# Kernel tuning notes

Measured on AMD Instinct MI355X. Metric: run time of the kernel, lower is better.

## Reference

```python
import jax, jax.numpy as jnp
import numpy as np
from jax import lax

NB, HH, WW, C = 8, 64, 64, 192
G, K, DW_K, PA_K = 12, 3, 5, 3
GC, P = C // G, K * K
PAD, STRIDE, DIL = 1, 1, 1
OFFSET_SCALE = 1.0
LN_EPS = 1e-5


def _grid_sample(img, grid):
    # img: (B,Cc,H,W); grid: (B,L,P,2) xy in [-1,1]; bilinear, zeros padding, align_corners=False
    B, Cc, H, W = img.shape
    gx = (grid[..., 0] + 1.0) * (W * 0.5) - 0.5
    gy = (grid[..., 1] + 1.0) * (H * 0.5) - 0.5
    x0, y0 = jnp.floor(gx), jnp.floor(gy)

    def gather(xi, yi):
        valid = (xi >= 0) & (xi <= W - 1) & (yi >= 0) & (yi <= H - 1)
        xc = jnp.clip(xi, 0, W - 1).astype(jnp.int32)
        yc = jnp.clip(yi, 0, H - 1).astype(jnp.int32)
        v = jax.vmap(lambda im, y, x: im[:, y, x])(img, yc, xc)  # (B,Cc,L,P)
        return v * valid[:, None].astype(img.dtype)

    wx1, wy1 = gx - x0, gy - y0
    wx0, wy0 = 1.0 - wx1, 1.0 - wy1
    return (gather(x0, y0) * (wx0 * wy0)[:, None]
            + gather(x0 + 1.0, y0) * (wx1 * wy0)[:, None]
            + gather(x0, y0 + 1.0) * (wx0 * wy1)[:, None]
            + gather(x0 + 1.0, y0 + 1.0) * (wx1 * wy1)[:, None])


def _dcnv3_core(x, offset, mask):
    # x: (N,H,W,C) projected input; offset: (N,H,W,G*P*2); mask: (N,H,W,G*P)
    N, H, W, _ = x.shape
    xp = jnp.pad(x, ((0, 0), (PAD, PAD), (PAD, PAD), (0, 0)))
    Hp, Wp = H + 2 * PAD, W + 2 * PAD
    Ho, Wo = offset.shape[1], offset.shape[2]
    base = (DIL * (K - 1)) // 2 + 0.5
    ref_y = (base + jnp.arange(Ho) * STRIDE) / Hp
    ref_x = (base + jnp.arange(Wo) * STRIDE) / Wp
    ref = jnp.stack(jnp.broadcast_arrays(ref_x[None, :], ref_y[:, None]), -1)  # (Ho,Wo,2) xy
    start = -((DIL * (K - 1)) // 2)
    pts = (start + jnp.arange(K) * DIL).astype(x.dtype)
    gxg = jnp.broadcast_to((pts / Wp)[:, None], (K, K))  # w offset varies along dim0 (torch order)
    gyg = jnp.broadcast_to((pts / Hp)[None, :], (K, K))
    grid = jnp.tile(jnp.stack([gxg, gyg], -1).reshape(P, 2), (G, 1))  # (G*P,2)
    loc = ref[None, :, :, None, :] + grid * OFFSET_SCALE  # (1,Ho,Wo,G*P,2)
    norm = jnp.array([Wp, Hp], dtype=x.dtype)
    loc = loc + offset.reshape(N, Ho, Wo, G * P, 2) * OFFSET_SCALE / norm
    sg = 2.0 * loc - 1.0  # (N,Ho,Wo,G*P,2)
    img = xp.reshape(N, Hp * Wp, G, GC).transpose(0, 2, 3, 1).reshape(N * G, GC, Hp, Wp)
    grd = sg.reshape(N, Ho * Wo, G, P, 2).transpose(0, 2, 1, 3, 4).reshape(N * G, Ho * Wo, P, 2)
    samp = _grid_sample(img, grd)  # (N*G, GC, L, P)
    m = mask.reshape(N, Ho * Wo, G, P).transpose(0, 2, 1, 3).reshape(N * G, 1, Ho * Wo, P)
    out = (samp * m).sum(-1)  # (N*G, GC, L)
    return out.reshape(N, G, GC, Ho * Wo).transpose(0, 3, 1, 2).reshape(N, Ho, Wo, C)


def _dcnv3(x, dw_w, dw_b, ln_g, ln_b, off_w, off_b, msk_w, msk_b, in_w, in_b, out_w, out_b, cfs_w, cfs_b):
    N, H, W, _ = x.shape
    x_proj = x @ in_w + in_b
    # depthwise conv (5x5) -> LayerNorm (channels_last) -> GELU(exact)
    u = lax.conv_general_dilated(x, dw_w, (1, 1), 'SAME',
                                 dimension_numbers=('NHWC', 'HWIO', 'NHWC'),
                                 feature_group_count=C) + dw_b
    mu = u.mean(-1, keepdims=True)
    var = ((u - mu) ** 2).mean(-1, keepdims=True)
    u = (u - mu) * lax.rsqrt(var + LN_EPS) * ln_g + ln_b
    u = jax.nn.gelu(u, approximate=False)
    offset = u @ off_w + off_b  # (N,H,W,G*P*2)
    m = jax.nn.softmax((u @ msk_w + msk_b).reshape(N, H, W, G, P), axis=-1).reshape(N, H, W, G * P)
    y = _dcnv3_core(x_proj, offset, m)
    cfs = jax.nn.sigmoid(u @ cfs_w + cfs_b)  # (N,H,W,G)
    cfs = jnp.repeat(cfs, GC, axis=-1)       # (N,H,W,C), group-blockwise
    y = y * (1.0 - cfs) + x_proj * cfs
    return y @ out_w + out_b


def _patch_attention(x):
    # x: (N,H,W,C) -> std over softmax'd 3x3 neighbor scores: (N,H,W)
    N, H, W, _ = x.shape
    pad = (PA_K - 1) // 2
    xp = jnp.pad(x, ((0, 0), (pad, pad), (pad, pad), (0, 0)))
    neigh = jnp.stack([xp[:, i:i + H, j:j + W, :] for i in range(PA_K) for j in range(PA_K)],
                      axis=-1)  # (N,H,W,C,K1*K2), torch unfold ordering
    scores = jnp.einsum('nhwc,nhwck->nhwk', x, neigh)
    sm = jax.nn.softmax(scores, axis=-1)
    return jnp.std(sm, axis=-1, ddof=1)  # torch.std is unbiased


def setup_inputs() -> dict:
    key = jax.random.key(0)
    ks = jax.random.split(key, 8)
    s = 0.02
    return {
        'x': jax.random.normal(ks[0], (NB, HH, WW, C), jnp.float32),
        'dw_w': jax.random.normal(ks[1], (DW_K, DW_K, 1, C), jnp.float32) * s,
        'dw_b': jnp.zeros((C,), jnp.float32),
        'ln_g': jnp.ones((C,), jnp.float32),
        'ln_b': jnp.zeros((C,), jnp.float32),
        'off_w': jax.random.normal(ks[2], (C, G * P * 2), jnp.float32) * s,
        'off_b': jnp.zeros((G * P * 2,), jnp.float32),
        'msk_w': jax.random.normal(ks[3], (C, G * P), jnp.float32) * s,
        'msk_b': jnp.zeros((G * P,), jnp.float32),
        'in_w': jax.random.normal(ks[4], (C, C), jnp.float32) * s,
        'in_b': jnp.zeros((C,), jnp.float32),
        'out_w': jax.random.normal(ks[5], (C, C), jnp.float32) * s,
        'out_b': jnp.zeros((C,), jnp.float32),
        'cfs_w': jax.random.normal(ks[6], (C, G), jnp.float32) * s,
        'cfs_b': jnp.zeros((G,), jnp.float32),
    }


def reference(x, dw_w, dw_b, ln_g, ln_b, off_w, off_b, msk_w, msk_b, in_w, in_b, out_w, out_b, cfs_w, cfs_b):
    x1 = _dcnv3(x, dw_w, dw_b, ln_g, ln_b, off_w, off_b, msk_w, msk_b, in_w, in_b, out_w, out_b, cfs_w, cfs_b)
    mask = _patch_attention(x1)           # (N,H,W)
    return x + x1 * mask[..., None]
```

## Files before the change

### kernel.cpp

```cpp
#include <hip/hip_runtime.h>
#include <hip/hip_bf16.h>
#include <math.h>

#define NB 8
#define HH 64
#define WW 64
#define C 192
#define G 12
#define GC 16
#define P 9
#define NPIX (NB*HH*WW)

typedef __attribute__((ext_vector_type(8))) short short8;
typedef __attribute__((ext_vector_type(4))) float f32x4;
typedef unsigned short ushort;

__device__ __forceinline__ ushort to_bf16(float f) {
  __hip_bfloat16 b = __float2bfloat16(f);
  return *(ushort*)&b;
}
__device__ __forceinline__ float bf2f(ushort u) {
  union { unsigned u; float f; } cv; cv.u = ((unsigned)u) << 16; return cv.f;
}
__device__ __forceinline__ float bflo(unsigned u) {
  union { unsigned v; float f; } c; c.v = u << 16; return c.f;
}
__device__ __forceinline__ float bfhi(unsigned u) {
  union { unsigned v; float f; } c; c.v = u & 0xffff0000u; return c.f;
}

__global__ void prep_w_kernel(const float* __restrict__ in_w, const float* __restrict__ out_w,
    const float* __restrict__ off_w, const float* __restrict__ msk_w, const float* __restrict__ cfs_w,
    const float* __restrict__ off_b, const float* __restrict__ msk_b, const float* __restrict__ cfs_b,
    ushort* __restrict__ in_wt, ushort* __restrict__ out_wt, ushort* __restrict__ wf_t,
    float* __restrict__ bf_bias) {
  int idx = blockIdx.x*256 + threadIdx.x;
  if (idx < 36864) {
    int n = idx/192, k = idx%192;
    in_wt[idx] = to_bf16(in_w[k*192 + n]);
  } else if (idx < 73728) {
    int j = idx - 36864; int n = j/192, k = j%192;
    out_wt[j] = to_bf16(out_w[k*192 + n]);
  } else if (idx < 147456) {
    int j = idx - 73728; int n = j/192, k = j%192;
    float v = 0.f;
    if (n < 216)      v = off_w[k*216 + n];
    else if (n < 324) v = msk_w[k*108 + (n-216)];
    else if (n < 336) v = cfs_w[k*12  + (n-324)];
    wf_t[j] = to_bf16(v);
  }
  if (idx < 384) {
    float b = 0.f;
    if (idx < 216)      b = off_b[idx];
    else if (idx < 324) b = msk_b[idx-216];
    else if (idx < 336) b = cfs_b[idx-324];
    bf_bias[idx] = b;
  }
}

template<int NW, int NSTORE, bool BF16OUT, bool AF32>
__global__ __launch_bounds__(256) void mfma_gemm(const void* __restrict__ A_,
    const ushort* __restrict__ Wt, const float* __restrict__ bias,
    void* __restrict__ Cout_) {
  __shared__ ushort As[4*128*8];
  __shared__ ushort Bs[4*64*8];
  int pix0 = blockIdx.x * 128, n0 = blockIdx.y * 64;
  int tid = threadIdx.x;
  int wid = tid >> 6, lane = tid & 63;
  int lr = lane >> 4, lc = lane & 15;

  f32x4 acc[2][4];
  #pragma unroll
  for (int m=0;m<2;m++)
    #pragma unroll
    for (int j=0;j<4;j++) acc[m][j] = (f32x4){0.f,0.f,0.f,0.f};

  int sa0_kb = tid >> 7,        sa0_row = tid & 127;
  int sa1_kb = (tid+256) >> 7,  sa1_row = (tid+256) & 127;
  int sb_kb  = tid >> 6,        sb_n    = tid & 63;

  short8 pa0, pa1, pb;
  auto load_tile = [&](int k0) {
    if (AF32) {
      const float* Af = (const float*)A_;
      float4 u0 = *(const float4*)&Af[(size_t)(pix0 + sa0_row)*192 + k0 + sa0_kb*8];
      float4 u1 = *(const float4*)&Af[(size_t)(pix0 + sa0_row)*192 + k0 + sa0_kb*8 + 4];
      pa0[0]=to_bf16(u0.x); pa0[1]=to_bf16(u0.y); pa0[2]=to_bf16(u0.z); pa0[3]=to_bf16(u0.w);
      pa0[4]=to_bf16(u1.x); pa0[5]=to_bf16(u1.y); pa0[6]=to_bf16(u1.z); pa0[7]=to_bf16(u1.w);
      float4 v0 = *(const float4*)&Af[(size_t)(pix0 + sa1_row)*192 + k0 + sa1_kb*8];
      float4 v1 = *(const float4*)&Af[(size_t)(pix0 + sa1_row)*192 + k0 + sa1_kb*8 + 4];
      pa1[0]=to_bf16(v0.x); pa1[1]=to_bf16(v0.y); pa1[2]=to_bf16(v0.z); pa1[3]=to_bf16(v0.w);
      pa1[4]=to_bf16(v1.x); pa1[5]=to_bf16(v1.y); pa1[6]=to_bf16(v1.z); pa1[7]=to_bf16(v1.w);
    } else {
      const ushort* Ab = (const ushort*)A_;
      pa0 = *(const short8*)&Ab[(size_t)(pix0 + sa0_row)*192 + k0 + sa0_kb*8];
      pa1 = *(const short8*)&Ab[(size_t)(pix0 + sa1_row)*192 + k0 + sa1_kb*8];
    }
    pb  = *(const short8*)&Wt[(size_t)(n0 + sb_n)*192 + k0 + sb_kb*8];
  };
  load_tile(0);

  for (int t = 0; t < 6; t++) {
    __syncthreads();
    *(short8*)&As[(size_t)tid*8]        = pa0;
    *(short8*)&As[(size_t)(tid+256)*8]  = pa1;
    *(short8*)&Bs[(size_t)tid*8]        = pb;
    __syncthreads();
    if (t < 5) load_tile((t+1)*32);
    short8 a0 = *(const short8*)&As[(size_t)(lr*128 + wid*32 + lc)*8];
    short8 a1 = *(const short8*)&As[(size_t)(lr*128 + wid*32 + 16 + lc)*8];
    #pragma unroll
    for (int j=0;j<4;j++) {
      short8 b = *(const short8*)&Bs[(size_t)(lr*64 + j*16 + lc)*8];
      acc[0][j] = __builtin_amdgcn_mfma_f32_16x16x32_bf16(a0, b, acc[0][j], 0,0,0);
      acc[1][j] = __builtin_amdgcn_mfma_f32_16x16x32_bf16(a1, b, acc[1][j], 0,0,0);
    }
  }
  #pragma unroll
  for (int j=0;j<4;j++) {
    int col = n0 + j*16 + lc;
    if (NW != NSTORE && col >= NSTORE) continue;
    float bb = bias[col];
    #pragma unroll
    for (int m=0;m<2;m++) {
      size_t rbase = pix0 + wid*32 + m*16 + lr*4;
      #pragma unroll
      for (int r=0;r<4;r++) {
        float v = acc[m][j][r] + bb;
        if (BF16OUT) ((ushort*)Cout_)[(rbase + r)*NSTORE + col] = to_bf16(v);
        else         ((float*) Cout_)[(rbase + r)*NSTORE + col] = v;
      }
    }
  }
}

#define SEG 16
__global__ __launch_bounds__(192) void dw_ln_gelu_kernel(const float* __restrict__ x,
    const float* __restrict__ dw_w, const float* __restrict__ dw_b,
    const float* __restrict__ ln_g, const float* __restrict__ ln_b,
    ushort* __restrict__ u_out) {
  int blk = blockIdx.x;
  int qw = blk & 3; int nh = blk >> 2;
  int h = nh & 63, n = nh >> 6;
  int c = threadIdx.x;
  int w0 = qw * SEG;

  float kw[25];
  #pragma unroll
  for (int t=0;t<25;t++) kw[t] = dw_w[t*C + c];

  float acc[SEG];
  float bb = dw_b[c];
  #pragma unroll
  for (int i=0;i<SEG;i++) acc[i] = bb;

  #pragma unroll
  for (int i=0;i<5;i++) {
    int hy = h + i - 2;
    if (hy < 0 || hy >= HH) continue;
    const float* rowp = &x[(((size_t)n*HH + hy)*WW)*C + c];
    #pragma unroll
    for (int wi=0; wi<SEG+4; wi++) {
      int w_in = w0 - 2 + wi;
      if (w_in < 0 || w_in >= WW) continue;
      float v = rowp[(size_t)w_in*C];
      #pragma unroll
      for (int j=0;j<5;j++) {
        int a = wi - j;
        if (a >= 0 && a < SEG) acc[a] += v * kw[i*5+j];
      }
    }
  }

  __shared__ float lds_acc[SEG][C+1];
  __shared__ float part1[SEG][12], part2[SEG][12];
  __shared__ float mu_s[SEG], rs_s[SEG];
  #pragma unroll
  for (int i=0;i<SEG;i++) lds_acc[i][c] = acc[i];
  __syncthreads();
  {
    int p = threadIdx.x & 15, chunk = threadIdx.x >> 4;
    float s1 = 0.f, s2 = 0.f;
    #pragma unroll
    for (int k=0;k<16;k++) {
      float v = lds_acc[p][chunk*16 + k];
      s1 += v; s2 += v*v;
    }
    part1[p][chunk] = s1; part2[p][chunk] = s2;
  }
  __syncthreads();
  if (threadIdx.x < SEG) {
    int p = threadIdx.x;
    float t1 = 0.f, t2 = 0.f;
    #pragma unroll
    for (int k=0;k<12;k++){ t1 += part1[p][k]; t2 += part2[p][k]; }
    float mu = t1 * (1.0f/C);
    float var = t2 * (1.0f/C) - mu*mu;
    mu_s[p] = mu; rs_s[p] = rsqrtf(var + 1e-5f);
  }
  __syncthreads();
  float gg = ln_g[c], lb = ln_b[c];
  size_t obase = ((size_t)nh*WW + w0)*C + c;
  #pragma unroll
  for (int i=0;i<SEG;i++) {
    float uv = (acc[i] - mu_s[i])*rs_s[i]*gg + lb;
    uv = 0.5f*uv*(1.0f + erff(uv*0.70710678118654752f));
    u_out[obase + (size_t)i*C] = to_bf16(uv);
  }
}

#define SPX 8
__device__ __forceinline__ void fma8(float* acc, float w, uint4 q) {
  acc[0] += w*bflo(q.x); acc[1] += w*bfhi(q.x);
  acc[2] += w*bflo(q.y); acc[3] += w*bfhi(q.y);
  acc[4] += w*bflo(q.z); acc[5] += w*bfhi(q.z);
  acc[6] += w*bflo(q.w); acc[7] += w*bfhi(q.w);
}
__global__ __launch_bounds__(192) void sample_kernel(const ushort* __restrict__ omc,
    const ushort* __restrict__ x_proj, ushort* __restrict__ y_out) {
  int pix0 = blockIdx.x * SPX;
  int n = pix0 >> 12;
  int hw = pix0 & 4095; int h = hw >> 6; int w0 = hw & 63;
  int tid = threadIdx.x;
  __shared__ int   addrs[SPX*108*4];
  __shared__ float wts[SPX*108*4];
  __shared__ float msm[SPX][108];
  __shared__ float cfss[SPX][12];

  for (int i = tid; i < SPX*108; i += 192) {
    int px = i / 108, gp = i % 108;
    int p = gp % 9;
    const float pts[3] = {-1.f, 0.f, 1.f};
    unsigned off2 = ((const unsigned*)omc)[(size_t)(pix0+px)*168 + gp];
    float ox = bflo(off2), oy = bfhi(off2);
    float gx = 1.0f + (float)(w0+px) + pts[p/3] + ox;
    float gy = 1.0f + (float)h + pts[p%3] + oy;
    float x0f = floorf(gx), y0f = floorf(gy);
    float wx1 = gx - x0f, wy1 = gy - y0f;
    float wx0 = 1.f-wx1, wy0 = 1.f-wy1;
    int x0 = (int)x0f, y0 = (int)y0f;
    bool xv0 = (x0   >= 1) && (x0   <= 64);
    bool xv1 = (x0+1 >= 1) && (x0+1 <= 64);
    bool yv0 = (y0   >= 1) && (y0   <= 64);
    bool yv1 = (y0+1 >= 1) && (y0+1 <= 64);
    int base = n*HH*WW*C;
    int4 a4;
    a4.x = (yv0&&xv0) ? (base + ((y0-1)*WW + (x0-1))*C)*2 : 0;
    a4.y = (yv0&&xv1) ? (base + ((y0-1)*WW + (x0  ))*C)*2 : 0;
    a4.z = (yv1&&xv0) ? (base + ((y0  )*WW + (x0-1))*C)*2 : 0;
    a4.w = (yv1&&xv1) ? (base + ((y0  )*WW + (x0  ))*C)*2 : 0;
    ((int4*)addrs)[i] = a4;
    float4 w4;
    w4.x = (yv0&&xv0) ? wx0*wy0 : 0.f;
    w4.y = (yv0&&xv1) ? wx1*wy0 : 0.f;
    w4.z = (yv1&&xv0) ? wx0*wy1 : 0.f;
    w4.w = (yv1&&xv1) ? wx1*wy1 : 0.f;
    ((float4*)wts)[i] = w4;
  }
  if (tid < SPX*12) {
    int px = tid / 12, gg = tid % 12;
    const ushort* mrow = &omc[(size_t)(pix0+px)*336 + 216 + gg*9];
    float lv[P];
    #pragma unroll
    for (int p=0;p<P;p++) lv[p] = bf2f(mrow[p]);
    float m = -1e30f;
    #pragma unroll
    for (int p=0;p<P;p++) m = fmaxf(m, lv[p]);
    float e[P]; float s = 0.f;
    #pragma unroll
    for (int p=0;p<P;p++){ e[p] = expf(lv[p]-m); s += e[p]; }
    float inv = 1.0f/s;
    #pragma unroll
    for (int p=0;p<P;p++) msm[px][gg*9+p] = e[p]*inv;
  } else {
    int q = tid - SPX*12;
    int px = q / 12, gg = q % 12;
    cfss[px][gg] = 1.0f/(1.0f+expf(-bf2f(omc[(size_t)(pix0+px)*336 + 324 + gg])));
  }
  __syncthreads();
  for (int i = tid; i < SPX*108; i += 192) {
    int px = i / 108, gp = i % 108;
    float m = msm[px][gp] * (1.0f - cfss[px][gp/9]);
    f32x4 w4 = *(f32x4*)&wts[i*4];
    w4 *= m;
    *(f32x4*)&wts[i*4] = w4;
  }
  __syncthreads();
  int px = tid / 24, s = tid - (tid/24)*24;
  int g = s >> 1;
  int cb = s * 16;
  const char* xb = (const char*)x_proj;
  float acc[8] = {0.f,0.f,0.f,0.f,0.f,0.f,0.f,0.f};
  #pragma unroll
  for (int pb = 0; pb < 3; pb++) {
    int gp = g*9 + pb*3;
    int4 a0 = ((const int4*)addrs)[px*108+gp];
    int4 a1 = ((const int4*)addrs)[px*108+gp+1];
    int4 a2 = ((const int4*)addrs)[px*108+gp+2];
    float4 wv0 = ((const float4*)wts)[px*108+gp];
    float4 wv1 = ((const float4*)wts)[px*108+gp+1];
    float4 wv2 = ((const float4*)wts)[px*108+gp+2];
    uint4 t00 = *(const uint4*)(xb + (unsigned)(a0.x + cb));
    uint4 t01 = *(const uint4*)(xb + (unsigned)(a0.y + cb));
    uint4 t02 = *(const uint4*)(xb + (unsigned)(a0.z + cb));
    uint4 t03 = *(const uint4*)(xb + (unsigned)(a0.w + cb));
    uint4 t10 = *(const uint4*)(xb + (unsigned)(a1.x + cb));
    uint4 t11 = *(const uint4*)(xb + (unsigned)(a1.y + cb));
    uint4 t12 = *(const uint4*)(xb + (unsigned)(a1.z + cb));
    uint4 t13 = *(const uint4*)(xb + (unsigned)(a1.w + cb));
    uint4 t20 = *(const uint4*)(xb + (unsigned)(a2.x + cb));
    uint4 t21 = *(const uint4*)(xb + (unsigned)(a2.y + cb));
    uint4 t22 = *(const uint4*)(xb + (unsigned)(a2.z + cb));
    uint4 t23 = *(const uint4*)(xb + (unsigned)(a2.w + cb));
    fma8(acc, wv0.x, t00); fma8(acc, wv0.y, t01);
    fma8(acc, wv0.z, t02); fma8(acc, wv0.w, t03);
    fma8(acc, wv1.x, t10); fma8(acc, wv1.y, t11);
    fma8(acc, wv1.z, t12); fma8(acc, wv1.w, t13);
    fma8(acc, wv2.x, t20); fma8(acc, wv2.y, t21);
    fma8(acc, wv2.z, t22); fma8(acc, wv2.w, t23);
  }
  float cf = cfss[px][g];
  uint4 qx = *(const uint4*)(xb + ((size_t)(pix0+px)*C)*2 + cb);
  fma8(acc, cf, qx);
  short8 r;
  #pragma unroll
  for (int k=0;k<8;k++) r[k] = to_bf16(acc[k]);
  *(short8*)&y_out[(size_t)(pix0+px)*C + s*8] = r;
}

__global__ __launch_bounds__(256) void pattn_kernel(const float* __restrict__ x,
    const ushort* __restrict__ x1, float* __restrict__ out) {
  __shared__ unsigned xs[100*97];
  __shared__ float psc[64][36];
  __shared__ float sd_s[64];
  int blk = blockIdx.x;
  int n = blk >> 6;
  int ty = (blk >> 3) & 7, tx = blk & 7;
  int th0 = ty*8, tw0 = tx*8;
  int tid = threadIdx.x;
  const unsigned* x1u = (const unsigned*)x1;
  for (int i = tid; i < 100*96; i += 256) {
    int cell = i / 96, wd = i - cell*96;
    int gy = th0 - 1 + cell/10, gx = tw0 - 1 + cell%10;
    unsigned v = 0;
    if (gy>=0 && gy<HH && gx>=0 && gx<WW)
      v = x1u[(((size_t)n*HH+gy)*WW+gx)*96 + wd];
    xs[cell*97 + wd] = v;
  }
  __syncthreads();
  {
    int px = tid >> 2, qq = tid & 3;
    int py = px >> 3, pxx = px & 7;
    int cell = (py+1)*10 + (pxx+1);
    float cen[48];
    #pragma unroll
    for (int k=0;k<24;k++) {
      unsigned w = xs[cell*97 + qq*24 + k];
      cen[2*k] = bflo(w); cen[2*k+1] = bfhi(w);
    }
    #pragma unroll
    for (int ni=0;ni<9;ni++) {
      int nc = cell + (ni/3-1)*10 + (ni%3-1);
      float a = 0.f;
      #pragma unroll
      for (int k=0;k<24;k++) {
        unsigned w = xs[nc*97 + qq*24 + k];
        a += cen[2*k]*bflo(w) + cen[2*k+1]*bfhi(w);
      }
      psc[px][qq*9+ni] = a;
    }
  }
  __syncthreads();
  if (tid < 64) {
    float sc[9];
    #pragma unroll
    for (int k=0;k<9;k++)
      sc[k] = psc[tid][k] + psc[tid][9+k] + psc[tid][18+k] + psc[tid][27+k];
    float m = sc[0];
    #pragma unroll
    for (int k=1;k<9;k++) m = fmaxf(m, sc[k]);
    float pr[9]; float s = 0.f;
    #pragma unroll
    for (int k=0;k<9;k++){ pr[k] = expf(sc[k]-m); s += pr[k]; }
    float inv = 1.0f/s;
    float mean = 0.f;
    #pragma unroll
    for (int k=0;k<9;k++){ pr[k] *= inv; mean += pr[k]; }
    mean *= (1.0f/9.0f);
    float var = 0.f;
    #pragma unroll
    for (int k=0;k<9;k++){ float d = pr[k]-mean; var += d*d; }
    sd_s[tid] = sqrtf(var*(1.0f/8.0f));
  }
  __syncthreads();
  for (int i = tid; i < 64*96; i += 256) {
    int p2 = i / 96, wd = i - p2*96;
    int py2 = p2 >> 3, px2 = p2 & 7;
    unsigned v = xs[((py2+1)*10 + (px2+1))*97 + wd];
    size_t pix = ((size_t)n*HH + th0+py2)*WW + tw0+px2;
    float2 xv = ((const float2*)x)[pix*96 + wd];
    float sd = sd_s[p2];
    float2 o; o.x = xv.x + bflo(v)*sd; o.y = xv.y + bfhi(v)*sd;
    ((float2*)out)[pix*96 + wd] = o;
  }
}

extern "C" void kernel_launch(void* const* d_in, const int* in_sizes, int n_in,
                              void* d_out, int out_size, void* d_ws, size_t ws_size,
                              hipStream_t stream) {
  const float* x     = (const float*)d_in[0];
  const float* dw_w  = (const float*)d_in[1];
  const float* dw_b  = (const float*)d_in[2];
  const float* ln_g  = (const float*)d_in[3];
  const float* ln_b  = (const float*)d_in[4];
  const float* off_w = (const float*)d_in[5];
  const float* off_b = (const float*)d_in[6];
  const float* msk_w = (const float*)d_in[7];
  const float* msk_b = (const float*)d_in[8];
  const float* in_w  = (const float*)d_in[9];
  const float* in_b  = (const float*)d_in[10];
  const float* out_w = (const float*)d_in[11];
  const float* out_b = (const float*)d_in[12];
  const float* cfs_w = (const float*)d_in[13];
  const float* cfs_b = (const float*)d_in[14];
  float* outp = (float*)d_out;

  ushort* omc    = (ushort*)d_ws;
  ushort* xproj  = omc + (size_t)NPIX*336;
  ushort* x1_bf  = xproj + (size_t)NPIX*192;
  ushort* u_bf   = x1_bf + (size_t)NPIX*192;
  ushort* in_wt  = u_bf + (size_t)NPIX*192;
  ushort* out_wt = in_wt + 192*192;
  ushort* wf_t   = out_wt + 192*192;
  float*  bfb    = (float*)(wf_t + 384*192);

  prep_w_kernel<<<(147456+255)/256, 256, 0, stream>>>(in_w, out_w, off_w, msk_w, cfs_w,
                                                       off_b, msk_b, cfs_b,
                                                       in_wt, out_wt, wf_t, bfb);
  mfma_gemm<192,192,true,true><<<dim3(NPIX/128, 3), 256, 0, stream>>>(x, in_wt, in_b, xproj);
  dw_ln_gelu_kernel<<<NB*HH*4, 192, 0, stream>>>(x, dw_w, dw_b, ln_g, ln_b, u_bf);
  mfma_gemm<384,336,true,false><<<dim3(NPIX/128, 6), 256, 0, stream>>>(u_bf, wf_t, bfb, omc);
  sample_kernel<<<NPIX/SPX, 192, 0, stream>>>(omc, xproj, u_bf);
  mfma_gemm<192,192,true,false><<<dim3(NPIX/128, 3), 256, 0, stream>>>(u_bf, out_wt, out_b, x1_bf);
  pattn_kernel<<<NB*64, 256, 0, stream>>>(x, x1_bf, outp);
}
```

Baseline: 155.3 us.

## Stage 8x8 tile halo of projected input in LDS for deformable sampling

The sampling kernel now works on 8x8 pixel tiles. Each block first loads a 12x12 halo of x_proj for all channels into shared memory, and the bilinear corner taps are read from there whenever they land inside the halo. Taps outside the halo fall back to global loads. Offset decoding, the mask softmax and the sigmoid weight are fused into the per-thread loop, which removes the separate shared-memory address and weight tables and two barriers. The cost is a large LDS footprint and a smaller grid (512 blocks), which may limit occupancy. It also adds a divergent fallback path when offsets are large.

```diff
diff --git a/kernel.cpp b/kernel.cpp
--- a/kernel.cpp
+++ b/kernel.cpp
@@ -209,123 +209,118 @@
   }
 }
 
-#define SPX 8
-__device__ __forceinline__ void fma8(float* acc, float w, uint4 q) {
-  acc[0] += w*bflo(q.x); acc[1] += w*bfhi(q.x);
-  acc[2] += w*bflo(q.y); acc[3] += w*bfhi(q.y);
-  acc[4] += w*bflo(q.z); acc[5] += w*bfhi(q.z);
-  acc[6] += w*bflo(q.w); acc[7] += w*bfhi(q.w);
-}
-__global__ __launch_bounds__(192) void sample_kernel(const ushort* __restrict__ omc,
+#define CELLB 400
+__device__ __forceinline__ void fma16(float* acc, float wv, uint4 q0, uint4 q1) {
+  acc[0] += wv*bflo(q0.x); acc[1] += wv*bfhi(q0.x);
+  acc[2] += wv*bflo(q0.y); acc[3] += wv*bfhi(q0.y);
+  acc[4] += wv*bflo(q0.z); acc[5] += wv*bfhi(q0.z);
+  acc[6] += wv*bflo(q0.w); acc[7] += wv*bfhi(q0.w);
+  acc[8]  += wv*bflo(q1.x); acc[9]  += wv*bfhi(q1.x);
+  acc[10] += wv*bflo(q1.y); acc[11] += wv*bfhi(q1.y);
+  acc[12] += wv*bflo(q1.z); acc[13] += wv*bfhi(q1.z);
+  acc[14] += wv*bflo(q1.w); acc[15] += wv*bfhi(q1.w);
+}
+__global__ __launch_bounds__(256) void sample_kernel(const ushort* __restrict__ omc,
     const ushort* __restrict__ x_proj, ushort* __restrict__ y_out) {
-  int pix0 = blockIdx.x * SPX;
-  int n = pix0 >> 12;
-  int hw = pix0 & 4095; int h = hw >> 6; int w0 = hw & 63;
+  __shared__ uint4 xs4[144*CELLB/16];
+  char* xs = (char*)xs4;
+  int blk = blockIdx.x;
+  int n = blk >> 6, ty = (blk >> 3) & 7, tx = blk & 7;
+  int h0 = ty*8, w0 = tx*8;
   int tid = threadIdx.x;
-  __shared__ int   addrs[SPX*108*4];
-  __shared__ float wts[SPX*108*4];
-  __shared__ float msm[SPX][108];
-  __shared__ float cfss[SPX][12];
-
-  for (int i = tid; i < SPX*108; i += 192) {
-    int px = i / 108, gp = i % 108;
-    int p = gp % 9;
-    const float pts[3] = {-1.f, 0.f, 1.f};
-    unsigned off2 = ((const unsigned*)omc)[(size_t)(pix0+px)*168 + gp];
-    float ox = bflo(off2), oy = bfhi(off2);
-    float gx = 1.0f + (float)(w0+px) + pts[p/3] + ox;
-    float gy = 1.0f + (float)h + pts[p%3] + oy;
-    float x0f = floorf(gx), y0f = floorf(gy);
-    float wx1 = gx - x0f, wy1 = gy - y0f;
-    float wx0 = 1.f-wx1, wy0 = 1.f-wy1;
-    int x0 = (int)x0f, y0 = (int)y0f;
-    bool xv0 = (x0   >= 1) && (x0   <= 64);
-    bool xv1 = (x0+1 >= 1) && (x0+1 <= 64);
-    bool yv0 = (y0   >= 1) && (y0   <= 64);
-    bool yv1 = (y0+1 >= 1) && (y0+1 <= 64);
-    int base = n*HH*WW*C;
-    int4 a4;
-    a4.x = (yv0&&xv0) ? (base + ((y0-1)*WW + (x0-1))*C)*2 : 0;
-    a4.y = (yv0&&xv1) ? (base + ((y0-1)*WW + (x0  ))*C)*2 : 0;
-    a4.z = (yv1&&xv0) ? (base + ((y0  )*WW + (x0-1))*C)*2 : 0;
-    a4.w = (yv1&&xv1) ? (base + ((y0  )*WW + (x0  ))*C)*2 : 0;
-    ((int4*)addrs)[i] = a4;
-    float4 w4;
-    w4.x = (yv0&&xv0) ? wx0*wy0 : 0.f;
-    w4.y = (yv0&&xv1) ? wx1*wy0 : 0.f;
-    w4.z = (yv1&&xv0) ? wx0*wy1 : 0.f;
-    w4.w = (yv1&&xv1) ? wx1*wy1 : 0.f;
-    ((float4*)wts)[i] = w4;
-  }
-  if (tid < SPX*12) {
-    int px = tid / 12, gg = tid % 12;
-    const ushort* mrow = &omc[(size_t)(pix0+px)*336 + 216 + gg*9];
-    float lv[P];
-    #pragma unroll
-    for (int p=0;p<P;p++) lv[p] = bf2f(mrow[p]);
-    float m = -1e30f;
-    #pragma unroll
-    for (int p=0;p<P;p++) m = fmaxf(m, lv[p]);
-    float e[P]; float s = 0.f;
-    #pragma unroll
-    for (int p=0;p<P;p++){ e[p] = expf(lv[p]-m); s += e[p]; }
-    float inv = 1.0f/s;
-    #pragma unroll
-    for (int p=0;p<P;p++) msm[px][gg*9+p] = e[p]*inv;
-  } else {
-    int q = tid - SPX*12;
-    int px = q / 12, gg = q % 12;
-    cfss[px][gg] = 1.0f/(1.0f+expf(-bf2f(omc[(size_t)(pix0+px)*336 + 324 + gg])));
-  }
-  __syncthreads();
-  for (int i = tid; i < SPX*108; i += 192) {
-    int px = i / 108, gp = i % 108;
-    float m = msm[px][gp] * (1.0f - cfss[px][gp/9]);
-    f32x4 w4 = *(f32x4*)&wts[i*4];
-    w4 *= m;
-    *(f32x4*)&wts[i*4] = w4;
-  }
-  __syncthreads();
-  int px = tid / 24, s = tid - (tid/24)*24;
-  int g = s >> 1;
-  int cb = s * 16;
+
+  for (int i = tid; i < 144*24; i += 256) {
+    int cell = i / 24, k = i - cell*24;
+    int r = cell / 12, c = cell - r*12;
+    int y_u = h0 + r - 2, x_u = w0 + c - 2;
+    uint4 v = {0u,0u,0u,0u};
+    if ((unsigned)y_u < 64u && (unsigned)x_u < 64u)
+      v = *(const uint4*)&x_proj[((size_t)n*4096 + y_u*64 + x_u)*192 + k*8];
+    *(uint4*)&xs[cell*CELLB + k*16] = v;
+  }
+  __syncthreads();
+
+  int px = tid >> 2, qq = tid & 3;
+  int py = px >> 3, pxx = px & 7;
+  int h = h0 + py, w = w0 + pxx;
+  size_t pix = (size_t)n*4096 + h*64 + w;
+  const unsigned* omc32 = (const unsigned*)omc;
   const char* xb = (const char*)x_proj;
-  float acc[8] = {0.f,0.f,0.f,0.f,0.f,0.f,0.f,0.f};
-  #pragma unroll
-  for (int pb = 0; pb < 3; pb++) {
-    int gp = g*9 + pb*3;
-    int4 a0 = ((const int4*)addrs)[px*108+gp];
-    int4 a1 = ((const int4*)addrs)[px*108+gp+1];
-    int4 a2 = ((const int4*)addrs)[px*108+gp+2];
-    float4 wv0 = ((const float4*)wts)[px*108+gp];
-    float4 wv1 = ((const float4*)wts)[px*108+gp+1];
-    float4 wv2 = ((const float4*)wts)[px*108+gp+2];
-    uint4 t00 = *(const uint4*)(xb + (unsigned)(a0.x + cb));
-    uint4 t01 = *(const uint4*)(xb + (unsigned)(a0.y + cb));
-    uint4 t02 = *(const uint4*)(xb + (unsigned)(a0.z + cb));
-    uint4 t03 = *(const uint4*)(xb + (unsigned)(a0.w + cb));
-    uint4 t10 = *(const uint4*)(xb + (unsigned)(a1.x + cb));
-    uint4 t11 = *(const uint4*)(xb + (unsigned)(a1.y + cb));
-    uint4 t12 = *(const uint4*)(xb + (unsigned)(a1.z + cb));
-    uint4 t13 = *(const uint4*)(xb + (unsigned)(a1.w + cb));
-    uint4 t20 = *(const uint4*)(xb + (unsigned)(a2.x + cb));
-    uint4 t21 = *(const uint4*)(xb + (unsigned)(a2.y + cb));
-    uint4 t22 = *(const uint4*)(xb + (unsigned)(a2.z + cb));
-    uint4 t23 = *(const uint4*)(xb + (unsigned)(a2.w + cb));
-    fma8(acc, wv0.x, t00); fma8(acc, wv0.y, t01);
-    fma8(acc, wv0.z, t02); fma8(acc, wv0.w, t03);
-    fma8(acc, wv1.x, t10); fma8(acc, wv1.y, t11);
-    fma8(acc, wv1.z, t12); fma8(acc, wv1.w, t13);
-    fma8(acc, wv2.x, t20); fma8(acc, wv2.y, t21);
-    fma8(acc, wv2.z, t22); fma8(acc, wv2.w, t23);
-  }
-  float cf = cfss[px][g];
-  uint4 qx = *(const uint4*)(xb + ((size_t)(pix0+px)*C)*2 + cb);
-  fma8(acc, cf, qx);
-  short8 r;
-  #pragma unroll
-  for (int k=0;k<8;k++) r[k] = to_bf16(acc[k]);
-  *(short8*)&y_out[(size_t)(pix0+px)*C + s*8] = r;
+  int mycell = (py+2)*12 + (pxx+2);
+  const float pts[3] = {-1.f, 0.f, 1.f};
+
+  for (int j = 0; j < 3; j++) {
+    int g = qq*3 + j;
+    int gch = g*32;
+    float lv[9];
+    #pragma unroll
+    for (int p=0;p<9;p++) lv[p] = bf2f(omc[pix*336 + 216 + g*9 + p]);
+    float mx = lv[0];
+    #pragma unroll
+    for (int p=1;p<9;p++) mx = fmaxf(mx, lv[p]);
+    float msum = 0.f;
+    #pragma unroll
+    for (int p=0;p<9;p++){ lv[p] = expf(lv[p]-mx); msum += lv[p]; }
+    float cf = 1.0f/(1.0f+expf(-bf2f(omc[pix*336 + 324 + g])));
+    float onemcf = (1.0f - cf) / msum;
+    float acc[16];
+    #pragma unroll
+    for (int k2=0;k2<16;k2++) acc[k2] = 0.f;
+
+    #pragma unroll
+    for (int p=0;p<9;p++) {
+      unsigned off2 = omc32[pix*168 + g*9 + p];
+      float ox = bflo(off2), oy = bfhi(off2);
+      float gx = 1.0f + (float)w + pts[p/3] + ox;
+      float gy = 1.0f + (float)h + pts[p%3] + oy;
+      float x0f = floorf(gx), y0f = floorf(gy);
+      float wx1 = gx-x0f, wy1 = gy-y0f;
+      float wx0 = 1.f-wx1, wy0 = 1.f-wy1;
+      int x0 = (int)x0f, y0 = (int)y0f;
+      int c0 = x0 - (w0-1), r0 = y0 - (h0-1);
+      float m = lv[p]*onemcf;
+      float w00 = wx0*wy0*m, w01 = wx1*wy0*m, w10 = wx0*wy1*m, w11 = wx1*wy1*m;
+      if ((unsigned)c0 <= 10u && (unsigned)r0 <= 10u) {
+        int b = (r0*12 + c0)*CELLB + gch;
+        uint4 qa0 = *(const uint4*)&xs[b],             qa1 = *(const uint4*)&xs[b+16];
+        uint4 qb0 = *(const uint4*)&xs[b+CELLB],       qb1 = *(const uint4*)&xs[b+CELLB+16];
+        uint4 qc0 = *(const uint4*)&xs[b+12*CELLB],    qc1 = *(const uint4*)&xs[b+12*CELLB+16];
+        uint4 qd0 = *(const uint4*)&xs[b+13*CELLB],    qd1 = *(const uint4*)&xs[b+13*CELLB+16];
+        fma16(acc, w00, qa0, qa1);
+        fma16(acc, w01, qb0, qb1);
+        fma16(acc, w10, qc0, qc1);
+        fma16(acc, w11, qd0, qd1);
+      } else {
+        bool xv0 = (x0>=1)&&(x0<=64), xv1 = (x0>=0)&&(x0<=63);
+        bool yv0 = (y0>=1)&&(y0<=64), yv1 = (y0>=0)&&(y0<=63);
+        int base = n*4096;
+        size_t ea = (yv0&&xv0) ? (size_t)(base + (y0-1)*64 + (x0-1))*384 : 0;
+        size_t eb = (yv0&&xv1) ? (size_t)(base + (y0-1)*64 + (x0  ))*384 : 0;
+        size_t ec = (yv1&&xv0) ? (size_t)(base + (y0  )*64 + (x0-1))*384 : 0;
+        size_t ed = (yv1&&xv1) ? (size_t)(base + (y0  )*64 + (x0  ))*384 : 0;
+        float wa = (yv0&&xv0)?w00:0.f, wb2 = (yv0&&xv1)?w01:0.f;
+        float wc = (yv1&&xv0)?w10:0.f, wd2 = (yv1&&xv1)?w11:0.f;
+        uint4 qa0 = *(const uint4*)(xb + ea + gch), qa1 = *(const uint4*)(xb + ea + gch + 16);
+        uint4 qb0 = *(const uint4*)(xb + eb + gch), qb1 = *(const uint4*)(xb + eb + gch + 16);
+        uint4 qc0 = *(const uint4*)(xb + ec + gch), qc1 = *(const uint4*)(xb + ec + gch + 16);
+        uint4 qd0 = *(const uint4*)(xb + ed + gch), qd1 = *(const uint4*)(xb + ed + gch + 16);
+        fma16(acc, wa, qa0, qa1);
+        fma16(acc, wb2, qb0, qb1);
+        fma16(acc, wc, qc0, qc1);
+        fma16(acc, wd2, qd0, qd1);
+      }
+    }
+    {
+      int b = mycell*CELLB + gch;
+      uint4 q0 = *(const uint4*)&xs[b], q1 = *(const uint4*)&xs[b+16];
+      fma16(acc, cf, q0, q1);
+    }
+    short8 r0v, r1v;
+    #pragma unroll
+    for (int k2=0;k2<8;k2++){ r0v[k2] = to_bf16(acc[k2]); r1v[k2] = to_bf16(acc[8+k2]); }
+    *(short8*)&y_out[pix*192 + g*16] = r0v;
+    *(short8*)&y_out[pix*192 + g*16 + 8] = r1v;
+  }
 }
 
 __global__ __launch_bounds__(256) void pattn_kernel(const float* __restrict__ x,
@@ -440,7 +435,7 @@
   mfma_gemm<192,192,true,true><<<dim3(NPIX/128, 3), 256, 0, stream>>>(x, in_wt, in_b, xproj);
   dw_ln_gelu_kernel<<<NB*HH*4, 192, 0, stream>>>(x, dw_w, dw_b, ln_g, ln_b, u_bf);
   mfma_gemm<384,336,true,false><<<dim3(NPIX/128, 6), 256, 0, stream>>>(u_bf, wf_t, bfb, omc);
-  sample_kernel<<<NPIX/SPX, 192, 0, stream>>>(omc, xproj, u_bf);
+  sample_kernel<<<NB*64, 256, 0, stream>>>(omc, xproj, u_bf);
   mfma_gemm<192,192,true,false><<<dim3(NPIX/128, 3), 256, 0, stream>>>(u_bf, out_wt, out_b, x1_bf);
   pattn_kernel<<<NB*64, 256, 0, stream>>>(x, x1_bf, outp);
 }
```

New measurement: 157.2 us. Within noise of the previous version (+1.3%).
